# Kernel tuning notes

Hardware: AMD Instinct MI355X
Metric: run time of the kernel (lower is better)

## Reference

```python
import jax, jax.numpy as jnp
import numpy as np

EPS_LN = 1e-6   # ln_1 / ln_2 (partial(LayerNorm, eps=1e-6))
EPS_ON = 1e-5   # SS2D out_norm (default LayerNorm eps)


def _ln(x, g, b, eps):
    m = jnp.mean(x, -1, keepdims=True)
    v = jnp.mean(jnp.square(x - m), -1, keepdims=True)
    return (x - m) * jax.lax.rsqrt(v + eps) * g + b


def _dwconv(x, w, b):
    # x: (B,C,H,W), w: (C,1,3,3) depthwise, 'SAME' padding (padding=1 for k=3)
    y = jax.lax.conv_general_dilated(x, w, (1, 1), 'SAME',
        feature_group_count=x.shape[1], dimension_numbers=('NCHW', 'OIHW', 'NCHW'))
    return y + b[None, :, None, None]


def _selective_scan(u, dts, A, Bs, Cs, Ds):
    # u, dts: (B,K,D,L); A: (K,D,N); Bs, Cs: (B,K,N,L); Ds: (K,D)
    B, K, D, L = u.shape
    N = A.shape[-1]
    uT = jnp.moveaxis(u, -1, 0)    # (L,B,K,D)
    dtT = jnp.moveaxis(dts, -1, 0)  # (L,B,K,D)
    BT = jnp.moveaxis(Bs, -1, 0)   # (L,B,K,N)
    CT = jnp.moveaxis(Cs, -1, 0)   # (L,B,K,N)

    def step(h, inp):
        u_t, dt_t, B_t, C_t = inp
        dA = jnp.exp(dt_t[..., None] * A)                                   # (B,K,D,N)
        h = dA * h + (dt_t * u_t)[..., None] * B_t[:, :, None, :]           # (B,K,D,N)
        y = jnp.einsum('bkdn,bkn->bkd', h, C_t)
        return h, y

    h0 = jnp.zeros((B, K, D, N), u.dtype)
    _, ys = jax.lax.scan(step, h0, (uT, dtT, BT, CT))
    ys = jnp.moveaxis(ys, 0, -1)   # (B,K,D,L)
    return ys + u * Ds[None, :, :, None]


def _ss2d(x, in_proj_w, conv_w, conv_b, x_proj_w, dt_w, dt_b, A_logs, Ds,
          onorm_g, onorm_b, out_proj_w):
    # x: (B,H,W,C) -> (B,H,W,C)
    B, H, W, C = x.shape
    Di = in_proj_w.shape[0] // 2
    K = x_proj_w.shape[0]
    R = dt_w.shape[-1]
    N = (x_proj_w.shape[1] - R) // 2
    L = H * W

    xz = x @ in_proj_w.T                       # (B,H,W,2*Di), bias=False
    xx, z = jnp.split(xz, 2, axis=-1)
    xx = jnp.transpose(xx, (0, 3, 1, 2))       # (B,Di,H,W)
    xx = jax.nn.silu(_dwconv(xx, conv_w, conv_b))

    # cross-scan: row-major, col-major, and their reversals
    x0 = xx.reshape(B, Di, L)
    x1 = jnp.transpose(xx, (0, 1, 3, 2)).reshape(B, Di, L)
    xs = jnp.stack([x0, x1, x0[..., ::-1], x1[..., ::-1]], axis=1)  # (B,K,Di,L)

    x_dbl = jnp.einsum('bkdl,kcd->bkcl', xs, x_proj_w)
    dts, Bs, Cs = jnp.split(x_dbl, [R, R + N], axis=2)
    dts = jnp.einsum('bkrl,kdr->bkdl', dts, dt_w)
    dts = jax.nn.softplus(dts + dt_b[None, :, :, None])
    A = -jnp.exp(A_logs.reshape(K, Di, N))

    ys = _selective_scan(xs, dts, A, Bs, Cs, Ds.reshape(K, Di))  # (B,K,Di,L)

    # cross-merge back to row-major
    y0 = ys[:, 0]
    y1 = jnp.transpose(ys[:, 1].reshape(B, Di, W, H), (0, 1, 3, 2)).reshape(B, Di, L)
    y2 = ys[:, 2, :, ::-1]
    y3 = jnp.transpose(ys[:, 3, :, ::-1].reshape(B, Di, W, H), (0, 1, 3, 2)).reshape(B, Di, L)
    y = jnp.transpose(y0 + y1 + y2 + y3, (0, 2, 1))              # (B,L,Di)
    y = _ln(y, onorm_g, onorm_b, EPS_ON).reshape(B, H, W, Di)
    y = y * jax.nn.silu(z)
    return y @ out_proj_w.T                    # bias=False


def setup_inputs() -> dict:
    key = jax.random.key(0)
    ks = jax.random.split(key, 16)
    B, H, W, C = 2, 56, 56, 192
    Di, N, K = 2 * C, 16, 4
    R = int(np.ceil(C / 16))                   # dt_rank = 12
    hid = 4 * C
    g = lambda k, shp, s=0.02: (jax.random.normal(k, shp) * s).astype(jnp.float32)
    return dict(
        x=jax.random.normal(ks[0], (B, H, W, C), jnp.float32),
        cpe1_w=g(ks[1], (C, 1, 3, 3), 0.1), cpe1_b=jnp.zeros((C,), jnp.float32),
        ln1_g=jnp.ones((C,), jnp.float32), ln1_b=jnp.zeros((C,), jnp.float32),
        in_proj_w=g(ks[2], (2 * Di, C)),
        conv_w=g(ks[3], (Di, 1, 3, 3), 0.1), conv_b=jnp.zeros((Di,), jnp.float32),
        x_proj_w=g(ks[4], (K, R + 2 * N, Di)),
        dt_w=g(ks[5], (K, Di, R), 0.1),
        dt_b=jnp.full((K, Di), float(np.log(np.expm1(0.01))), jnp.float32),
        A_logs=jnp.log(jnp.tile(jnp.arange(1, N + 1, dtype=jnp.float32), (K * Di, 1))),
        Ds=jnp.ones((K * Di,), jnp.float32),
        onorm_g=jnp.ones((Di,), jnp.float32), onorm_b=jnp.zeros((Di,), jnp.float32),
        out_proj_w=g(ks[6], (C, Di)),
        cpe2_w=g(ks[7], (C, 1, 3, 3), 0.1), cpe2_b=jnp.zeros((C,), jnp.float32),
        ln2_g=jnp.ones((C,), jnp.float32), ln2_b=jnp.zeros((C,), jnp.float32),
        fc1_w=g(ks[8], (hid, C)), fc1_b=jnp.zeros((hid,), jnp.float32),
        fc2_w=g(ks[9], (C, hid)), fc2_b=jnp.zeros((C,), jnp.float32),
    )


def reference(x, cpe1_w, cpe1_b, ln1_g, ln1_b, in_proj_w, conv_w, conv_b,
              x_proj_w, dt_w, dt_b, A_logs, Ds, onorm_g, onorm_b, out_proj_w,
              cpe2_w, cpe2_b, ln2_g, ln2_b, fc1_w, fc1_b, fc2_w, fc2_b):
    # x: (B,H,W,C)
    x = x + jnp.transpose(_dwconv(jnp.transpose(x, (0, 3, 1, 2)), cpe1_w, cpe1_b), (0, 2, 3, 1))
    x = x + _ss2d(_ln(x, ln1_g, ln1_b, EPS_LN), in_proj_w, conv_w, conv_b,
                  x_proj_w, dt_w, dt_b, A_logs, Ds, onorm_g, onorm_b, out_proj_w)
    x = x + jnp.transpose(_dwconv(jnp.transpose(x, (0, 3, 1, 2)), cpe2_w, cpe2_b), (0, 2, 3, 1))
    h = _ln(x, ln2_g, ln2_b, EPS_LN)
    h = jax.nn.gelu(h @ fc1_w.T + fc1_b, approximate=False)
    x = x + (h @ fc2_w.T + fc2_b)
    return x
```

## Files before the change

### kernel.cpp

```cpp
#include <hip/hip_runtime.h>
#include <math.h>

#define BB 2
#define HHH 56
#define WWW 56
#define CC 192
#define LL 3136
#define DI 384
#define KK 4
#define NN 16
#define RR 12
#define CP 44
#define HIDN 768
#define BL (BB*LL)
#define NCH 98
#define CHL 32

typedef __attribute__((ext_vector_type(8))) short bf16x8;
typedef __attribute__((ext_vector_type(4))) float f32x4;

__device__ __forceinline__ float siluf_(float x){ return x/(1.f+__expf(-x)); }
__device__ __forceinline__ float geluf_(float x){ return 0.5f*x*(1.f+erff(x*0.70710678118654752f)); }
__device__ __forceinline__ unsigned short bf16r_(float x){
  unsigned int u = __float_as_uint(x);
  u += 0x7FFFu + ((u>>16)&1u);
  return (unsigned short)(u>>16);
}
__device__ __forceinline__ float bf2f_(unsigned short u){
  return __uint_as_float(((unsigned int)u)<<16);
}

__global__ void k_prep(const float* __restrict__ s0, const float* __restrict__ s1,
                       const float* __restrict__ s2, const float* __restrict__ s3,
                       unsigned short* __restrict__ dst,
                       const float* __restrict__ xp, unsigned short* __restrict__ wXhi,
                       unsigned short* __restrict__ wXlo){
  if (blockIdx.x < 2016){
    int i = blockIdx.x*256 + threadIdx.x;
    if      (i < 147456) dst[i] = bf16r_(s0[i]);
    else if (i < 221184) dst[i] = bf16r_(s1[i-147456]);
    else if (i < 368640) dst[i] = bf16r_(s2[i-221184]);
    else if (i < 516096) dst[i] = bf16r_(s3[i-368640]);
  } else {
    int idx = (blockIdx.x-2016)*256 + threadIdx.x;
    if (idx >= 192*384) return;
    int row = idx / 384, d = idx % 384;
    int k = row / 48, j = row % 48;
    float v = 0.f;
    if (j < 12) v = xp[(k*CP + j)*DI + d];
    else if (j >= 16) v = xp[(k*CP + (j-4))*DI + d];
    unsigned short hi = bf16r_(v);
    wXhi[idx] = hi;
    wXlo[idx] = bf16r_(v - bf2f_(hi));
  }
}

__global__ void k_dwconv_res(const float* __restrict__ in, const float* __restrict__ wgt,
                             const float* __restrict__ bias, float* __restrict__ out) {
  int idx = blockIdx.x*256 + threadIdx.x;
  const int total = BB*HHH*WWW*CC;
  if (idx >= total) return;
  int c = idx % CC;
  int w = (idx / CC) % WWW;
  int h = (idx / (CC*WWW)) % HHH;
  int b = idx / (CC*WWW*HHH);
  float acc = bias[c];
  #pragma unroll
  for (int kh=0; kh<3; kh++){
    int hh = h + kh - 1; if (hh < 0 || hh >= HHH) continue;
    #pragma unroll
    for (int kw=0; kw<3; kw++){
      int ww = w + kw - 1; if (ww < 0 || ww >= WWW) continue;
      acc += in[((b*HHH+hh)*WWW+ww)*CC + c] * wgt[c*9 + kh*3 + kw];
    }
  }
  out[idx] = in[idx] + acc;
}

__global__ void k_ln192(const float* __restrict__ in, const float* __restrict__ g,
                        const float* __restrict__ bta, unsigned short* __restrict__ out, float eps) {
  int row = blockIdx.x*4 + (threadIdx.x>>6);
  int lane = threadIdx.x & 63;
  const float* p = in + (size_t)row*CC;
  float v0=p[lane], v1=p[lane+64], v2=p[lane+128];
  float s = v0+v1+v2, s2 = v0*v0+v1*v1+v2*v2;
  #pragma unroll
  for (int off=1; off<64; off<<=1){ s += __shfl_xor(s,off); s2 += __shfl_xor(s2,off); }
  float m = s*(1.f/192.f);
  float var = s2*(1.f/192.f) - m*m;
  float rstd = rsqrtf(var + eps);
  unsigned short* q = out + (size_t)row*CC;
  q[lane]     = bf16r_((v0-m)*rstd*g[lane]     + bta[lane]);
  q[lane+64]  = bf16r_((v1-m)*rstd*g[lane+64]  + bta[lane+64]);
  q[lane+128] = bf16r_((v2-m)*rstd*g[lane+128] + bta[lane+128]);
}

enum { EPI_NONE=0, EPI_RES=1, EPI_BIAS_GELU=2, EPI_BIAS_RES=3 };

template<int MT, int EPI, int OUTBF>
__global__ __launch_bounds__(256) void k_gemm_mfma(const unsigned short* __restrict__ A,
      const unsigned short* __restrict__ W, const float* __restrict__ bias,
      const float* __restrict__ res, void* __restrict__ outp, int M, int Nn, int Kk) {
  __shared__ unsigned short As[MT][40];
  __shared__ unsigned short Bs[64][40];
  constexpr int NI = (MT==128) ? 4 : 2;
  int tid = threadIdx.x;
  int m0 = blockIdx.y*MT, n0 = blockIdx.x*64;
  int wid = tid>>6, lane = tid&63;
  int wm = (MT==128) ? wid*32 : (wid&1)*32;
  int wn = (MT==128) ? 0 : (wid>>1)*32;
  int fr = lane&15, fk = (lane>>4)*8;
  f32x4 acc[2][NI];
  #pragma unroll
  for (int i=0;i<2;i++)
    #pragma unroll
    for (int j=0;j<NI;j++) acc[i][j] = (f32x4){0.f,0.f,0.f,0.f};
  int arow, ak;
  if (MT==128){ arow = tid>>1; ak = (tid&1)*16; }
  else        { arow = tid>>2; ak = (tid&3)*8;  }
  int wrow = tid>>2, wk = (tid&3)*8;
  const unsigned short* Ap = A + (size_t)(m0+arow)*Kk + ak;
  const unsigned short* Wp = W + (size_t)(n0+wrow)*Kk + wk;
  for (int k0=0; k0<Kk; k0+=32){
    __syncthreads();
    if (MT==128){
      uint4 av0 = *(const uint4*)(Ap + k0);
      uint4 av1 = *(const uint4*)(Ap + k0 + 8);
      *(uint4*)&As[arow][ak]   = av0;
      *(uint4*)&As[arow][ak+8] = av1;
    } else {
      *(uint4*)&As[arow][ak] = *(const uint4*)(Ap + k0);
    }
    *(uint4*)&Bs[wrow][wk] = *(const uint4*)(Wp + k0);
    __syncthreads();
    bf16x8 af[2], bfr[NI];
    #pragma unroll
    for (int mi=0;mi<2;mi++) af[mi] = *(const bf16x8*)&As[wm + mi*16 + fr][fk];
    #pragma unroll
    for (int ni=0;ni<NI;ni++) bfr[ni] = *(const bf16x8*)&Bs[wn + ni*16 + fr][fk];
    #pragma unroll
    for (int mi=0;mi<2;mi++)
      #pragma unroll
      for (int ni=0;ni<NI;ni++)
        acc[mi][ni] = __builtin_amdgcn_mfma_f32_16x16x32_bf16(af[mi], bfr[ni], acc[mi][ni], 0,0,0);
  }
  int rbase = (lane>>4)*4;
  #pragma unroll
  for (int mi=0;mi<2;mi++){
    #pragma unroll
    for (int ni=0;ni<NI;ni++){
      int col = n0 + wn + ni*16 + fr;
      float bv = (EPI==EPI_BIAS_GELU || EPI==EPI_BIAS_RES) ? bias[col] : 0.f;
      #pragma unroll
      for (int r=0;r<4;r++){
        int row = m0 + wm + mi*16 + rbase + r;
        float v = acc[mi][ni][r] + bv;
        if (EPI==EPI_BIAS_GELU) v = geluf_(v);
        if (EPI==EPI_RES || EPI==EPI_BIAS_RES) v += res[(size_t)row*Nn + col];
        if (OUTBF) ((unsigned short*)outp)[(size_t)row*Nn + col] = bf16r_(v);
        else       ((float*)outp)[(size_t)row*Nn + col] = v;
      }
    }
  }
}

__global__ __launch_bounds__(256) void k_xgemm(const float* __restrict__ uf,
      const unsigned short* __restrict__ wXhi, const unsigned short* __restrict__ wXlo,
      float* __restrict__ xdblT) {
  __shared__ unsigned short Ah[64][40];
  __shared__ unsigned short Al[64][40];
  __shared__ unsigned short Bh[64][40];
  __shared__ unsigned short Bl[64][40];
  int tid = threadIdx.x;
  int m0 = blockIdx.y*64, n0 = blockIdx.x*64;
  int wid = tid>>6, lane = tid&63;
  int fr = lane&15, fk = (lane>>4)*8;
  f32x4 acc[4];
  #pragma unroll
  for (int j=0;j<4;j++) acc[j] = (f32x4){0.f,0.f,0.f,0.f};
  int srow = tid>>2, sk = (tid&3)*8;
  const float* Ap = uf + (size_t)(m0+srow)*DI + sk;
  const unsigned short* Wh = wXhi + (size_t)(n0+srow)*DI + sk;
  const unsigned short* Wl = wXlo + (size_t)(n0+srow)*DI + sk;
  for (int k0=0; k0<DI; k0+=32){
    __syncthreads();
    float4 ua = *(const float4*)(Ap + k0);
    float4 ub = *(const float4*)(Ap + k0 + 4);
    uint4 wh = *(const uint4*)(Wh + k0);
    uint4 wl = *(const uint4*)(Wl + k0);
    float uv[8] = {ua.x,ua.y,ua.z,ua.w, ub.x,ub.y,ub.z,ub.w};
    #pragma unroll
    for (int j=0;j<8;j++){
      unsigned short hi = bf16r_(uv[j]);
      Ah[srow][sk+j] = hi;
      Al[srow][sk+j] = bf16r_(uv[j] - bf2f_(hi));
    }
    *(uint4*)&Bh[srow][sk] = wh;
    *(uint4*)&Bl[srow][sk] = wl;
    __syncthreads();
    bf16x8 ah = *(const bf16x8*)&Ah[wid*16 + fr][fk];
    bf16x8 al = *(const bf16x8*)&Al[wid*16 + fr][fk];
    #pragma unroll
    for (int ni=0;ni<4;ni++){
      bf16x8 bh = *(const bf16x8*)&Bh[ni*16 + fr][fk];
      bf16x8 bl = *(const bf16x8*)&Bl[ni*16 + fr][fk];
      acc[ni] = __builtin_amdgcn_mfma_f32_16x16x32_bf16(ah, bh, acc[ni], 0,0,0);
      acc[ni] = __builtin_amdgcn_mfma_f32_16x16x32_bf16(al, bh, acc[ni], 0,0,0);
      acc[ni] = __builtin_amdgcn_mfma_f32_16x16x32_bf16(ah, bl, acc[ni], 0,0,0);
    }
  }
  int rbase = (lane>>4)*4;
  #pragma unroll
  for (int ni=0;ni<4;ni++){
    int col = n0 + ni*16 + fr;
    int k = col / 48, j = col % 48;
    #pragma unroll
    for (int r=0;r<4;r++){
      int row = m0 + wid*16 + rbase + r;
      int b = row / LL, s = row % LL;
      int h = s / WWW, w2 = s % WWW;
      int l1 = w2*HHH + h;
      int lk = (k==0) ? s : (k==1) ? l1 : (k==2) ? (LL-1-s) : (LL-1-l1);
      xdblT[((size_t)((b*KK+k)*LL + lk))*48 + j] = acc[ni][r];
    }
  }
}

__global__ void k_conv_xx(const float* __restrict__ xz, const float* __restrict__ cw,
                          const float* __restrict__ cb, float* __restrict__ xc0,
                          float* __restrict__ xc1) {
  int idx = blockIdx.x*256 + threadIdx.x;
  if (idx >= BB*LL*DI) return;
  int d = idx % DI;
  int l = (idx / DI) % LL;
  int b = idx / (DI*LL);
  int h = l / WWW, w = l % WWW;
  float acc = cb[d];
  #pragma unroll
  for (int kh=0; kh<3; kh++){
    int hh = h + kh - 1; if (hh < 0 || hh >= HHH) continue;
    #pragma unroll
    for (int kw=0; kw<3; kw++){
      int ww2 = w + kw - 1; if (ww2 < 0 || ww2 >= WWW) continue;
      acc += xz[((size_t)(b*LL + hh*WWW + ww2))*(2*DI) + d] * cw[d*9 + kh*3 + kw];
    }
  }
  float v = siluf_(acc);
  xc0[idx] = v;
  xc1[((size_t)(b*LL + w*HHH + h))*DI + d] = v;
}

template<int PASS>
__global__ __launch_bounds__(64) void k_scan(const float* __restrict__ xc_l0,
        const float* __restrict__ xc_l1,
        const float* __restrict__ xdblT, const float* __restrict__ dtw, const float* __restrict__ dtb,
        const float* __restrict__ alogs, const float* __restrict__ Dsv,
        unsigned short* __restrict__ hend, float* __restrict__ sumdt, unsigned short* __restrict__ ysb) {
  __shared__ float recs[CHL*48];
  __shared__ float us[CHL][64];
  int ch = blockIdx.y, bk = blockIdx.z;
  int b = bk >> 2, k = bk & 3;
  int lane = threadIdx.x;
  int d = blockIdx.x*64 + lane;
  int kd = k*DI + d;
  const float* usrc = (k & 1) ? xc_l1 : xc_l0;
  bool rev = (k >= 2);
  const float4* rg = (const float4*)(xdblT + ((size_t)bk*LL + ch*CHL)*48);
  float4* rs = (float4*)recs;
  #pragma unroll
  for (int j=0;j<6;j++) rs[lane + j*64] = rg[lane + j*64];
  #pragma unroll
  for (int j=0;j<CHL;j++){
    int li = ch*CHL + j;
    int lsrc = rev ? (LL-1-li) : li;
    us[j][lane] = usrc[((size_t)(b*LL + lsrc))*DI + d];
  }
  float w[12];
  #pragma unroll
  for (int r=0;r<12;r++) w[r] = dtw[kd*12 + r];
  float biasd = dtb[kd];
  float Dd = (PASS==1) ? Dsv[kd] : 0.f;
  float An2[16];
  #pragma unroll
  for (int n=0;n<16;n++) An2[n] = -__expf(alogs[kd*16 + n]) * 1.44269504f;
  bool pw = true;
  #pragma unroll
  for (int n=1;n<16;n++) pw = pw && (fabsf(An2[n] - (float)(n+1)*An2[0]) <= 1e-3f*(float)(n+1)*fabsf(An2[0]));
  float h[16];
  size_t hb = ((size_t)(bk*NCH + ch)*DI + d)*16;
  if (PASS==0){
    #pragma unroll
    for (int n=0;n<16;n++) h[n]=0.f;
  } else {
    uint4 q0 = *(const uint4*)&hend[hb];
    uint4 q1 = *(const uint4*)&hend[hb+8];
    unsigned int qa[8] = {q0.x,q0.y,q0.z,q0.w, q1.x,q1.y,q1.z,q1.w};
    #pragma unroll
    for (int j=0;j<8;j++){
      h[2*j]   = bf2f_((unsigned short)(qa[j] & 0xffffu));
      h[2*j+1] = bf2f_((unsigned short)(qa[j] >> 16));
    }
  }
  __syncthreads();
  float cum = 0.f;
  #pragma unroll 2
  for (int i=0;i<CHL;i++){
    int li = ch*CHL + i;
    float uu = us[i][lane];
    const float* rec = recs + i*48;
    float4 t0 = *(const float4*)(rec);
    float4 t1 = *(const float4*)(rec+4);
    float4 t2 = *(const float4*)(rec+8);
    float4 B0 = *(const float4*)(rec+16);
    float4 B1 = *(const float4*)(rec+20);
    float4 B2 = *(const float4*)(rec+24);
    float4 B3 = *(const float4*)(rec+28);
    float a0 = fmaf(t0.x,w[0], fmaf(t0.y,w[1], fmaf(t0.z,w[2], t0.w*w[3])));
    float a1 = fmaf(t1.x,w[4], fmaf(t1.y,w[5], fmaf(t1.z,w[6], t1.w*w[7])));
    float a2 = fmaf(t2.x,w[8], fmaf(t2.y,w[9], fmaf(t2.z,w[10], t2.w*w[11])));
    float a = biasd + a0 + (a1 + a2);
    float dt = 0.69314718f * log2f(1.f + exp2f(a*1.44269504f));
    float dtu = dt*uu;
    if (PASS==0) cum += dt;
    float dA[16];
    if (pw){
      float r1 = exp2f(dt*An2[0]);
      float r2 = r1*r1;
      float r3 = r2*r1;
      float r4 = r2*r2;
      float r8 = r4*r4;
      dA[0]=r1;     dA[1]=r2;     dA[2]=r3;     dA[3]=r4;
      dA[4]=r4*r1;  dA[5]=r4*r2;  dA[6]=r4*r3;  dA[7]=r8;
      dA[8]=r8*r1;  dA[9]=r8*r2;  dA[10]=r8*r3; dA[11]=r8*r4;
      dA[12]=r8*dA[4]; dA[13]=r8*dA[5]; dA[14]=r8*dA[6]; dA[15]=r8*r8;
    } else {
      #pragma unroll
      for (int n=0;n<16;n++) dA[n] = exp2f(dt*An2[n]);
    }
    float Bv[16] = {B0.x,B0.y,B0.z,B0.w, B1.x,B1.y,B1.z,B1.w,
                    B2.x,B2.y,B2.z,B2.w, B3.x,B3.y,B3.z,B3.w};
    #pragma unroll
    for (int n=0;n<16;n++) h[n] = fmaf(dA[n], h[n], dtu*Bv[n]);
    if (PASS==1){
      float4 C0 = *(const float4*)(rec+32);
      float4 C1 = *(const float4*)(rec+36);
      float4 C2 = *(const float4*)(rec+40);
      float4 C3 = *(const float4*)(rec+44);
      float y0 = fmaf(h[0], C0.x, fmaf(h[1], C0.y, fmaf(h[2], C0.z, h[3]*C0.w)));
      float y1 = fmaf(h[4], C1.x, fmaf(h[5], C1.y, fmaf(h[6], C1.z, h[7]*C1.w)));
      float y2 = fmaf(h[8], C2.x, fmaf(h[9], C2.y, fmaf(h[10],C2.z, h[11]*C2.w)));
      float y3 = fmaf(h[12],C3.x, fmaf(h[13],C3.y, fmaf(h[14],C3.z, h[15]*C3.w)));
      float y = fmaf(uu, Dd, (y0+y1)+(y2+y3));
      ysb[((size_t)(bk*LL + li))*DI + d] = bf16r_(y);
    }
  }
  if (PASS==0){
    unsigned int pk[8];
    #pragma unroll
    for (int j=0;j<8;j++)
      pk[j] = ((unsigned int)bf16r_(h[2*j+1])<<16) | (unsigned int)bf16r_(h[2*j]);
    *(uint4*)&hend[hb]   = make_uint4(pk[0],pk[1],pk[2],pk[3]);
    *(uint4*)&hend[hb+8] = make_uint4(pk[4],pk[5],pk[6],pk[7]);
    sumdt[(bk*NCH + ch)*DI + d] = cum;
  }
}

__global__ __launch_bounds__(64) void k_scanmid(const float* __restrict__ alogs,
        const float* __restrict__ sumdt, unsigned short* __restrict__ hend) {
  int bid = blockIdx.x;
  int dblk = bid % 96;
  int k = (bid/96) % KK;
  int b = bid/(96*KK);
  int lane = threadIdx.x;
  int d4 = lane>>4, n = lane&15;
  int d = dblk*4 + d4;
  int bk = b*KK + k;
  float Ac2 = -__expf(alogs[(k*DI+d)*16 + n]) * 1.44269504f;
  float H = 0.f;
  for (int c=0;c<NCH;c++){
    float sdt = sumdt[(bk*NCH + c)*DI + d];
    float aexp = exp2f(Ac2 * sdt);
    size_t idx = ((size_t)(bk*NCH + c)*DI + dblk*4)*16 + lane;
    float tmp = bf2f_(hend[idx]);
    hend[idx] = bf16r_(H);
    H = fmaf(aexp, H, tmp);
  }
}

__global__ __launch_bounds__(384) void k_fuse(const unsigned short* __restrict__ ysb,
      const float* __restrict__ xz, const float* __restrict__ og, const float* __restrict__ ob,
      unsigned short* __restrict__ a2) {
  __shared__ float sa[6], sb[6];
  int b = blockIdx.x / LL, l = blockIdx.x % LL;
  int d = threadIdx.x;
  int h_ = l / WWW, w_ = l % WWW;
  int l1 = w_*HHH + h_;
  float y = bf2f_(ysb[((size_t)((b*KK+0)*LL + l))*DI + d])
          + bf2f_(ysb[((size_t)((b*KK+1)*LL + l1))*DI + d])
          + bf2f_(ysb[((size_t)((b*KK+2)*LL + (LL-1-l)))*DI + d])
          + bf2f_(ysb[((size_t)((b*KK+3)*LL + (LL-1-l1)))*DI + d]);
  float s = y, s2 = y*y;
  #pragma unroll
  for (int off=1; off<64; off<<=1){ s += __shfl_xor(s,off); s2 += __shfl_xor(s2,off); }
  int wid = d >> 6;
  if ((d & 63) == 0){ sa[wid] = s; sb[wid] = s2; }
  __syncthreads();
  s = sa[0]+sa[1]+sa[2]+sa[3]+sa[4]+sa[5];
  s2 = sb[0]+sb[1]+sb[2]+sb[3]+sb[4]+sb[5];
  float m = s*(1.f/DI);
  float var = s2*(1.f/DI) - m*m;
  float rstd = rsqrtf(var + 1e-5f);
  float v = (y - m)*rstd*og[d] + ob[d];
  float z = xz[((size_t)(b*LL + l))*(2*DI) + DI + d];
  a2[((size_t)(b*LL + l))*DI + d] = bf16r_(v * siluf_(z));
}

extern "C" void kernel_launch(void* const* d_in, const int* in_sizes, int n_in,
                              void* d_out, int out_size, void* d_ws, size_t ws_size,
                              hipStream_t stream) {
  (void)in_sizes; (void)n_in; (void)out_size; (void)ws_size;
  const float* x       = (const float*)d_in[0];
  const float* cpe1_w  = (const float*)d_in[1];
  const float* cpe1_b  = (const float*)d_in[2];
  const float* ln1_g   = (const float*)d_in[3];
  const float* ln1_b   = (const float*)d_in[4];
  const float* in_proj = (const float*)d_in[5];
  const float* conv_w  = (const float*)d_in[6];
  const float* conv_b  = (const float*)d_in[7];
  const float* x_proj  = (const float*)d_in[8];
  const float* dt_w    = (const float*)d_in[9];
  const float* dt_b    = (const float*)d_in[10];
  const float* A_logs  = (const float*)d_in[11];
  const float* Dsv     = (const float*)d_in[12];
  const float* onorm_g = (const float*)d_in[13];
  const float* onorm_b = (const float*)d_in[14];
  const float* out_proj= (const float*)d_in[15];
  const float* cpe2_w  = (const float*)d_in[16];
  const float* cpe2_b  = (const float*)d_in[17];
  const float* ln2_g   = (const float*)d_in[18];
  const float* ln2_b   = (const float*)d_in[19];
  const float* fc1_w   = (const float*)d_in[20];
  const float* fc1_b   = (const float*)d_in[21];
  const float* fc2_w   = (const float*)d_in[22];
  const float* fc2_b   = (const float*)d_in[23];
  float* out = (float*)d_out;
  float* wsf = (float*)d_ws;

  float* x1    = wsf;
  float* xlnf  = x1 + 1204224;
  float* xz    = xlnf + 1204224;
  float* xc_l0 = xz + 4816896;
  float* xc_l1 = xc_l0 + 2408448;
  float* ysbf  = xc_l1 + 2408448;
  float* hendf = ysbf + 4816896;
  float* sumdt = hendf + 2408448;
  float* xdblT = sumdt + 301056;
  unsigned short* wbf = (unsigned short*)(xdblT + 1204224);
  unsigned short* wXhi = wbf + 516096;
  unsigned short* wXlo = wXhi + 73728;
  unsigned short* xln  = (unsigned short*)xlnf;
  unsigned short* xln2 = (unsigned short*)xlnf;
  unsigned short* ysb  = (unsigned short*)ysbf;
  unsigned short* hend = (unsigned short*)hendf;
  unsigned short* a2   = (unsigned short*)xdblT;
  float* x2   = xc_l0;
  float* x3   = xz;
  unsigned short* hbuf = (unsigned short*)ysbf;
  unsigned short* wIn  = wbf;
  unsigned short* wOut = wbf + 147456;
  unsigned short* wF1  = wbf + 221184;
  unsigned short* wF2  = wbf + 368640;

  k_prep<<<2016+288, 256, 0, stream>>>(in_proj, out_proj, fc1_w, fc2_w, wbf, x_proj, wXhi, wXlo);
  k_dwconv_res<<<(BB*HHH*WWW*CC+255)/256, 256, 0, stream>>>(x, cpe1_w, cpe1_b, x1);
  k_ln192<<<BL/4, 256, 0, stream>>>(x1, ln1_g, ln1_b, xln, 1e-6f);
  k_gemm_mfma<128,EPI_NONE,0><<<dim3(768/64, BL/128), 256, 0, stream>>>(xln, wIn, nullptr, nullptr, xz, BL, 2*DI, CC);
  k_conv_xx<<<(BB*LL*DI+255)/256, 256, 0, stream>>>(xz, conv_w, conv_b, xc_l0, xc_l1);
  k_xgemm<<<dim3(3, BL/64), 256, 0, stream>>>(xc_l0, wXhi, wXlo, xdblT);
  k_scan<0><<<dim3(6, NCH, BB*KK), 64, 0, stream>>>(xc_l0, xc_l1, xdblT, dt_w, dt_b, A_logs, Dsv, hend, sumdt, ysb);
  k_scanmid<<<BB*KK*96, 64, 0, stream>>>(A_logs, sumdt, hend);
  k_scan<1><<<dim3(6, NCH, BB*KK), 64, 0, stream>>>(xc_l0, xc_l1, xdblT, dt_w, dt_b, A_logs, Dsv, hend, sumdt, ysb);
  k_fuse<<<BB*LL, 384, 0, stream>>>(ysb, xz, onorm_g, onorm_b, a2);
  k_gemm_mfma<64,EPI_RES,0><<<dim3(192/64, BL/64), 256, 0, stream>>>(a2, wOut, nullptr, x1, x2, BL, CC, DI);
  k_dwconv_res<<<(BB*HHH*WWW*CC+255)/256, 256, 0, stream>>>(x2, cpe2_w, cpe2_b, x3);
  k_ln192<<<BL/4, 256, 0, stream>>>(x3, ln2_g, ln2_b, xln2, 1e-6f);
  k_gemm_mfma<128,EPI_BIAS_GELU,1><<<dim3(768/64, BL/128), 256, 0, stream>>>(xln2, wF1, fc1_b, nullptr, hbuf, BL, HIDN, CC);
  k_gemm_mfma<64,EPI_BIAS_RES,0><<<dim3(192/64, BL/64), 256, 0, stream>>>(hbuf, wF2, fc2_b, x3, out, BL, CC, HIDN);
}
```

Measured before the change: 239.3 us.

## Fuse depthwise conv residual with LayerNorm; stream scan inputs directly from global

Merges the depthwise-conv-plus-residual kernel and the following LayerNorm into one kernel, with one block per pixel and 192 threads, reducing across wavefronts through shared memory. This removes a launch and a re-read of the intermediate activation. Separately, the scan kernel no longer stages the u values into shared memory before the loop and instead loads them from global memory inside the recurrence. That shortens the prologue and frees shared memory, but it puts global-load latency inside the serial loop.

```diff
diff --git a/kernel.cpp b/kernel.cpp
--- a/kernel.cpp
+++ b/kernel.cpp
@@ -55,15 +55,14 @@
   }
 }
 
-__global__ void k_dwconv_res(const float* __restrict__ in, const float* __restrict__ wgt,
-                             const float* __restrict__ bias, float* __restrict__ out) {
-  int idx = blockIdx.x*256 + threadIdx.x;
-  const int total = BB*HHH*WWW*CC;
-  if (idx >= total) return;
-  int c = idx % CC;
-  int w = (idx / CC) % WWW;
-  int h = (idx / (CC*WWW)) % HHH;
-  int b = idx / (CC*WWW*HHH);
+__global__ __launch_bounds__(192) void k_dwln(const float* __restrict__ in,
+      const float* __restrict__ wgt, const float* __restrict__ bias,
+      const float* __restrict__ g, const float* __restrict__ bta,
+      float* __restrict__ xout, unsigned short* __restrict__ lnout, float eps) {
+  __shared__ float sa[3], sb[3];
+  int pix = blockIdx.x;
+  int c = threadIdx.x;
+  int w = pix % WWW, h = (pix/WWW) % HHH, b = pix/(WWW*HHH);
   float acc = bias[c];
   #pragma unroll
   for (int kh=0; kh<3; kh++){
@@ -74,25 +73,20 @@
       acc += in[((b*HHH+hh)*WWW+ww)*CC + c] * wgt[c*9 + kh*3 + kw];
     }
   }
-  out[idx] = in[idx] + acc;
-}
-
-__global__ void k_ln192(const float* __restrict__ in, const float* __restrict__ g,
-                        const float* __restrict__ bta, unsigned short* __restrict__ out, float eps) {
-  int row = blockIdx.x*4 + (threadIdx.x>>6);
-  int lane = threadIdx.x & 63;
-  const float* p = in + (size_t)row*CC;
-  float v0=p[lane], v1=p[lane+64], v2=p[lane+128];
-  float s = v0+v1+v2, s2 = v0*v0+v1*v1+v2*v2;
+  float v = in[(size_t)pix*CC + c] + acc;
+  xout[(size_t)pix*CC + c] = v;
+  float s = v, s2 = v*v;
   #pragma unroll
   for (int off=1; off<64; off<<=1){ s += __shfl_xor(s,off); s2 += __shfl_xor(s2,off); }
+  int wv = c >> 6;
+  if ((c & 63) == 0){ sa[wv] = s; sb[wv] = s2; }
+  __syncthreads();
+  s = sa[0]+sa[1]+sa[2];
+  s2 = sb[0]+sb[1]+sb[2];
   float m = s*(1.f/192.f);
   float var = s2*(1.f/192.f) - m*m;
   float rstd = rsqrtf(var + eps);
-  unsigned short* q = out + (size_t)row*CC;
-  q[lane]     = bf16r_((v0-m)*rstd*g[lane]     + bta[lane]);
-  q[lane+64]  = bf16r_((v1-m)*rstd*g[lane+64]  + bta[lane+64]);
-  q[lane+128] = bf16r_((v2-m)*rstd*g[lane+128] + bta[lane+128]);
+  lnout[(size_t)pix*CC + c] = bf16r_((v-m)*rstd*g[c] + bta[c]);
 }
 
 enum { EPI_NONE=0, EPI_RES=1, EPI_BIAS_GELU=2, EPI_BIAS_RES=3 };
@@ -257,24 +251,15 @@
         const float* __restrict__ alogs, const float* __restrict__ Dsv,
         unsigned short* __restrict__ hend, float* __restrict__ sumdt, unsigned short* __restrict__ ysb) {
   __shared__ float recs[CHL*48];
-  __shared__ float us[CHL][64];
   int ch = blockIdx.y, bk = blockIdx.z;
   int b = bk >> 2, k = bk & 3;
   int lane = threadIdx.x;
   int d = blockIdx.x*64 + lane;
   int kd = k*DI + d;
-  const float* usrc = (k & 1) ? xc_l1 : xc_l0;
-  bool rev = (k >= 2);
   const float4* rg = (const float4*)(xdblT + ((size_t)bk*LL + ch*CHL)*48);
   float4* rs = (float4*)recs;
   #pragma unroll
   for (int j=0;j<6;j++) rs[lane + j*64] = rg[lane + j*64];
-  #pragma unroll
-  for (int j=0;j<CHL;j++){
-    int li = ch*CHL + j;
-    int lsrc = rev ? (LL-1-li) : li;
-    us[j][lane] = usrc[((size_t)(b*LL + lsrc))*DI + d];
-  }
   float w[12];
   #pragma unroll
   for (int r=0;r<12;r++) w[r] = dtw[kd*12 + r];
@@ -286,6 +271,8 @@
   bool pw = true;
   #pragma unroll
   for (int n=1;n<16;n++) pw = pw && (fabsf(An2[n] - (float)(n+1)*An2[0]) <= 1e-3f*(float)(n+1)*fabsf(An2[0]));
+  const float* usrc = (k & 1) ? xc_l1 : xc_l0;
+  bool rev = (k >= 2);
   float h[16];
   size_t hb = ((size_t)(bk*NCH + ch)*DI + d)*16;
   if (PASS==0){
@@ -306,7 +293,8 @@
   #pragma unroll 2
   for (int i=0;i<CHL;i++){
     int li = ch*CHL + i;
-    float uu = us[i][lane];
+    int lsrc = rev ? (LL-1-li) : li;
+    float uu = usrc[((size_t)(b*LL + lsrc))*DI + d];
     const float* rec = recs + i*48;
     float4 t0 = *(const float4*)(rec);
     float4 t1 = *(const float4*)(rec+4);
@@ -472,8 +460,7 @@
   unsigned short* wF2  = wbf + 368640;
 
   k_prep<<<2016+288, 256, 0, stream>>>(in_proj, out_proj, fc1_w, fc2_w, wbf, x_proj, wXhi, wXlo);
-  k_dwconv_res<<<(BB*HHH*WWW*CC+255)/256, 256, 0, stream>>>(x, cpe1_w, cpe1_b, x1);
-  k_ln192<<<BL/4, 256, 0, stream>>>(x1, ln1_g, ln1_b, xln, 1e-6f);
+  k_dwln<<<BB*HHH*WWW, 192, 0, stream>>>(x, cpe1_w, cpe1_b, ln1_g, ln1_b, x1, xln, 1e-6f);
   k_gemm_mfma<128,EPI_NONE,0><<<dim3(768/64, BL/128), 256, 0, stream>>>(xln, wIn, nullptr, nullptr, xz, BL, 2*DI, CC);
   k_conv_xx<<<(BB*LL*DI+255)/256, 256, 0, stream>>>(xz, conv_w, conv_b, xc_l0, xc_l1);
   k_xgemm<<<dim3(3, BL/64), 256, 0, stream>>>(xc_l0, wXhi, wXlo, xdblT);
@@ -482,8 +469,7 @@
   k_scan<1><<<dim3(6, NCH, BB*KK), 64, 0, stream>>>(xc_l0, xc_l1, xdblT, dt_w, dt_b, A_logs, Dsv, hend, sumdt, ysb);
   k_fuse<<<BB*LL, 384, 0, stream>>>(ysb, xz, onorm_g, onorm_b, a2);
   k_gemm_mfma<64,EPI_RES,0><<<dim3(192/64, BL/64), 256, 0, stream>>>(a2, wOut, nullptr, x1, x2, BL, CC, DI);
-  k_dwconv_res<<<(BB*HHH*WWW*CC+255)/256, 256, 0, stream>>>(x2, cpe2_w, cpe2_b, x3);
-  k_ln192<<<BL/4, 256, 0, stream>>>(x3, ln2_g, ln2_b, xln2, 1e-6f);
+  k_dwln<<<BB*HHH*WWW, 192, 0, stream>>>(x2, cpe2_w, cpe2_b, ln2_g, ln2_b, x3, xln2, 1e-6f);
   k_gemm_mfma<128,EPI_BIAS_GELU,1><<<dim3(768/64, BL/128), 256, 0, stream>>>(xln2, wF1, fc1_b, nullptr, hbuf, BL, HIDN, CC);
   k_gemm_mfma<64,EPI_BIAS_RES,0><<<dim3(192/64, BL/64), 256, 0, stream>>>(hbuf, wF2, fc2_b, x3, out, BL, CC, HIDN);
 }
```

After: 217.1 us. -9.3%, faster.
